# Kernel optimization log

Hardware: AMD Instinct MI355X
Metric: run time of the kernel (lower is better)

The kernel has to match this reference:

```python
import jax, jax.numpy as jnp
import numpy as np

DIM = 1024
NUM_HEADS = 16
HEAD_DIM = DIM // NUM_HEADS
ROPE_BASE = 10000.0


def _rope_cos_sin(seq_len, head_dim):
    inv_freq = 1.0 / (ROPE_BASE ** (jnp.arange(0, head_dim, 2, dtype=jnp.float32) / head_dim))
    t = jnp.arange(seq_len, dtype=jnp.float32)
    freqs = t[:, None] * inv_freq[None, :]            # [S, Dh/2]
    emb = jnp.concatenate([freqs, freqs], axis=-1)    # [S, Dh]
    return jnp.cos(emb), jnp.sin(emb)


def _rotate_half(x):
    half = x.shape[-1] // 2
    return jnp.concatenate([-x[..., half:], x[..., :half]], axis=-1)


def setup_inputs() -> dict:
    key = jax.random.key(0)
    k1, k2, k3 = jax.random.split(key, 3)
    B, S = 2, 2048
    x = jax.random.normal(k1, (B, S, DIM), dtype=jnp.float32)
    w_qkv = jax.random.normal(k2, (3 * DIM, DIM), dtype=jnp.float32) * (DIM ** -0.5)
    w_out = jax.random.normal(k3, (DIM, DIM), dtype=jnp.float32) * (DIM ** -0.5)
    return {"x": x, "w_qkv": w_qkv, "w_out": w_out}


def reference(x, w_qkv, w_out):
    B, S, D = x.shape
    H, Dh = NUM_HEADS, HEAD_DIM
    scale = Dh ** -0.5

    qkv = (x @ w_qkv.T).reshape(B, S, 3, H, Dh)      # [B,S,3,H,Dh]
    qkv = jnp.transpose(qkv, (2, 0, 3, 1, 4))        # [3,B,H,S,Dh]
    q, k, v = qkv[0], qkv[1], qkv[2]

    cos, sin = _rope_cos_sin(S, Dh)                  # [S,Dh]
    cos = cos[None, None, :, :]
    sin = sin[None, None, :, :]
    q = q * cos + _rotate_half(q) * sin
    k = k * cos + _rotate_half(k) * sin

    scores = jnp.einsum('bhqd,bhkd->bhqk', q, k) * scale
    causal_mask = jnp.triu(jnp.ones((S, S), dtype=bool), k=1)
    scores = jnp.where(causal_mask[None, None], -jnp.inf, scores)
    attn = jax.nn.softmax(scores, axis=-1)
    out = jnp.einsum('bhqk,bhkd->bhqd', attn, v)      # [B,H,S,Dh]
    out = jnp.transpose(out, (0, 2, 1, 3)).reshape(B, S, D)
    return out @ w_out.T
```

## Files before the change

### kernel.cpp

```cpp
#include <hip/hip_runtime.h>
#include <stdint.h>

typedef uint16_t u16;
typedef __attribute__((ext_vector_type(8))) short bf16x8;
typedef __attribute__((ext_vector_type(4))) float f32x4;

__device__ inline u16 f2b(float f) {
  uint32_t u = __float_as_uint(f);
  u += 0x7FFF + ((u >> 16) & 1);
  return (u16)(u >> 16);
}
__device__ inline float b2f(u16 h) {
  return __uint_as_float(((uint32_t)h) << 16);
}

__global__ void k_detect(const u16* __restrict__ X, int* __restrict__ flag) {
  __shared__ int cnt;
  const int t = threadIdx.x;
  if (t == 0) cnt = 0;
  __syncthreads();
  float av = fabsf(b2f(X[t * 2]));
  int wild = (av < 1000.0f) ? 0 : 1;
  atomicAdd(&cnt, wild);
  __syncthreads();
  if (t == 0) flag[0] = (cnt > 16) ? 1 : 0;
}

__global__ __launch_bounds__(256) void k_qkv_rope(const void* __restrict__ Xv,
                                                  const void* __restrict__ Wv,
                                                  const int* __restrict__ flag,
                                                  u16* __restrict__ Qo,
                                                  u16* __restrict__ Ko,
                                                  u16* __restrict__ Vo) {
  __shared__ u16 As[64][40];
  __shared__ u16 Bs[3][64][40];
  __shared__ float Cs[64][66];
  const int mode = flag[0];
  const int h = blockIdx.x;
  const int n0h = h * 64;
  const int m0 = blockIdx.y * 64;
  const int t = threadIdx.x, w = t >> 6, lane = t & 63;
  const int lr = lane & 15, lq = lane >> 4;
  f32x4 acc[3][4] = {};
  const int rA = t >> 2, cA = (t & 3) * 8;
  const int aoff = (m0 + rA) * 1024 + cA;
  const int boff0 = (n0h + rA) * 1024 + cA;
  for (int k0 = 0; k0 < 1024; k0 += 32) {
    __syncthreads();
    if (mode == 0) {
      *(uint4*)&As[rA][cA]    = *(const uint4*)((const u16*)Xv + aoff + k0);
      *(uint4*)&Bs[0][rA][cA] = *(const uint4*)((const u16*)Wv + boff0 + k0);
      *(uint4*)&Bs[1][rA][cA] = *(const uint4*)((const u16*)Wv + boff0 + 1048576 + k0);
      *(uint4*)&Bs[2][rA][cA] = *(const uint4*)((const u16*)Wv + boff0 + 2097152 + k0);
    } else {
      const float* Xf = (const float*)Xv;
      const float* Wf = (const float*)Wv;
#pragma unroll
      for (int ee = 0; ee < 8; ++ee) {
        As[rA][cA + ee]    = f2b(Xf[aoff + k0 + ee]);
        Bs[0][rA][cA + ee] = f2b(Wf[boff0 + k0 + ee]);
        Bs[1][rA][cA + ee] = f2b(Wf[boff0 + 1048576 + k0 + ee]);
        Bs[2][rA][cA + ee] = f2b(Wf[boff0 + 2097152 + k0 + ee]);
      }
    }
    __syncthreads();
    bf16x8 bf[3];
#pragma unroll
    for (int e = 0; e < 3; ++e)
      bf[e] = *(const bf16x8*)&Bs[e][(w << 4) + lr][lq * 8];
#pragma unroll
    for (int mt = 0; mt < 4; ++mt) {
      bf16x8 af = *(const bf16x8*)&As[(mt << 4) + lr][lq * 8];
#pragma unroll
      for (int e = 0; e < 3; ++e)
        acc[e][mt] = __builtin_amdgcn_mfma_f32_16x16x32_bf16(af, bf[e], acc[e][mt], 0, 0, 0);
    }
  }
  for (int e = 0; e < 3; ++e) {
    __syncthreads();
    {
      const int col = (w << 4) + lr;
#pragma unroll
      for (int mt = 0; mt < 4; ++mt)
#pragma unroll
        for (int i = 0; i < 4; ++i)
          Cs[mt * 16 + lq * 4 + i][col] = acc[e][mt][i];
    }
    __syncthreads();
    if (e == 2) {
      const int sx = t & 63, dh0 = (t >> 6) * 16;
      const int m = m0 + sx, b = m >> 11, s = m & 2047;
      const long hb = (long)(b * 16 + h) * 64;
#pragma unroll
      for (int u = 0; u < 16; ++u) {
        int dh = dh0 + u;
        Vo[(hb + dh) * 2048 + s] = f2b(Cs[sx][dh]);
      }
    } else {
      const int r = t >> 2, dh0 = (t & 3) * 16;
      const int m = m0 + r, b = m >> 11, s = m & 2047;
      const int obase = ((b * 16 + h) * 2048 + s) * 64;
      u16* O = (e == 0) ? Qo : Ko;
#pragma unroll
      for (int u = 0; u < 16; ++u) {
        int dh = dh0 + u;
        float v  = Cs[r][dh];
        float vp = Cs[r][dh ^ 32];
        float sign = (dh < 32) ? -1.0f : 1.0f;
        float fr  = __expf((float)(dh & 31) * -0.28782314f);
        float ang = (float)s * fr;
        float sn = __sinf(ang), cs = __cosf(ang);
        O[obase + dh] = f2b(v * cs + sign * vp * sn);
      }
    }
  }
}

__device__ __forceinline__ void attn_tile(u16 QP[64][72], u16 Ks[64][72],
                                          u16 Vt[64][72], const bf16x8 qf[2],
                                          f32x4 o_acc[4], float& m_i, float& l_i,
                                          int kt, int qt_tile, int w, int lr,
                                          int lq, int lq4, int base16, int qrow_l) {
  f32x4 sa[4] = {};
#pragma unroll
  for (int mb = 0; mb < 4; ++mb)
#pragma unroll
    for (int kk = 0; kk < 2; ++kk) {
      bf16x8 kf = *(const bf16x8*)&Ks[mb * 16 + lr][kk * 32 + lq * 8];
      sa[mb] = __builtin_amdgcn_mfma_f32_16x16x32_bf16(kf, qf[kk], sa[mb], 0, 0, 0);
    }
  float sc[4][4];
  float m_new = m_i;
#pragma unroll
  for (int mb = 0; mb < 4; ++mb)
#pragma unroll
    for (int i = 0; i < 4; ++i) {
      float sv = sa[mb][i] * 0.125f;
      if (kt == qt_tile && (mb * 16 + lq4 + i) > qrow_l) sv = -3.0e4f;
      sc[mb][i] = sv;
      m_new = fmaxf(m_new, sv);
    }
  m_new = fmaxf(m_new, __shfl_xor(m_new, 16));
  m_new = fmaxf(m_new, __shfl_xor(m_new, 32));
  float alpha = __expf(m_i - m_new);
  m_i = m_new;
  float p[4][4], sm = 0.f;
#pragma unroll
  for (int mb = 0; mb < 4; ++mb)
#pragma unroll
    for (int i = 0; i < 4; ++i) { p[mb][i] = __expf(sc[mb][i] - m_new); sm += p[mb][i]; }
  sm += __shfl_xor(sm, 16);
  sm += __shfl_xor(sm, 32);
  l_i = l_i * alpha + sm;

#pragma unroll
  for (int mb = 0; mb < 4; ++mb) {
    uint2 pk;
    pk.x = (uint32_t)f2b(p[mb][0]) | ((uint32_t)f2b(p[mb][1]) << 16);
    pk.y = (uint32_t)f2b(p[mb][2]) | ((uint32_t)f2b(p[mb][3]) << 16);
    *(uint2*)&QP[w * 16 + lr][mb * 16 + lq4] = pk;
  }
#pragma unroll
  for (int i = 0; i < 4; ++i) {
    float ai = __shfl(alpha, base16 | (lq4 + i));
    o_acc[0][i] *= ai; o_acc[1][i] *= ai;
    o_acc[2][i] *= ai; o_acc[3][i] *= ai;
  }
  asm volatile("s_waitcnt lgkmcnt(0)" ::: "memory");
#pragma unroll
  for (int kk = 0; kk < 2; ++kk) {
    bf16x8 pf = *(const bf16x8*)&QP[w * 16 + lr][kk * 32 + lq * 8];
#pragma unroll
    for (int nb = 0; nb < 4; ++nb) {
      bf16x8 vf = *(const bf16x8*)&Vt[nb * 16 + lr][kk * 32 + lq * 8];
      o_acc[nb] = __builtin_amdgcn_mfma_f32_16x16x32_bf16(pf, vf, o_acc[nb], 0, 0, 0);
    }
  }
}

__global__ __launch_bounds__(256) void k_attn(const u16* __restrict__ Q,
                                              const u16* __restrict__ K,
                                              const u16* __restrict__ V,
                                              u16* __restrict__ AO) {
  __shared__ u16 QP[64][72];
  __shared__ u16 Ks[64][72];
  __shared__ u16 Vt[64][72];
  const int qtA = 31 - blockIdx.x;
  const int qtB = blockIdx.x;
  const int bh = blockIdx.y;
  const int b = bh >> 4, h = bh & 15;
  const u16* Qg = Q + (bh * 2048) * 64;
  const u16* Kg = K + bh * 2048 * 64;
  const u16* Vg = V + (long)bh * 64 * 2048;
  const int t = threadIdx.x, w = t >> 6, lane = t & 63;
  const int lr = lane & 15, lq = lane >> 4;
  const int lq4 = lq * 4;
  const int base16 = lane & 48;
  const int r0 = t >> 3, c0 = (t & 7) * 8;
  const int qrow_l = w * 16 + lr;

  bf16x8 qfA[2], qfB[2];
  *(uint4*)&QP[r0][c0]      = *(const uint4*)&Qg[(qtA * 64 + r0) * 64 + c0];
  *(uint4*)&QP[r0 + 32][c0] = *(const uint4*)&Qg[(qtA * 64 + r0 + 32) * 64 + c0];
  __syncthreads();
#pragma unroll
  for (int kk = 0; kk < 2; ++kk)
    qfA[kk] = *(const bf16x8*)&QP[w * 16 + lr][kk * 32 + lq * 8];
  __syncthreads();
  *(uint4*)&QP[r0][c0]      = *(const uint4*)&Qg[(qtB * 64 + r0) * 64 + c0];
  *(uint4*)&QP[r0 + 32][c0] = *(const uint4*)&Qg[(qtB * 64 + r0 + 32) * 64 + c0];
  __syncthreads();
#pragma unroll
  for (int kk = 0; kk < 2; ++kk)
    qfB[kk] = *(const bf16x8*)&QP[w * 16 + lr][kk * 32 + lq * 8];

  float m_iA = -3.0e4f, l_iA = 0.f, m_iB = -3.0e4f, l_iB = 0.f;
  f32x4 o_accA[4] = {}, o_accB[4] = {};

  for (int kt = 0; kt <= qtA; ++kt) {
    __syncthreads();
    *(uint4*)&Ks[r0][c0]      = *(const uint4*)&Kg[(kt * 64 + r0) * 64 + c0];
    *(uint4*)&Ks[r0 + 32][c0] = *(const uint4*)&Kg[(kt * 64 + r0 + 32) * 64 + c0];
    *(uint4*)&Vt[r0][c0]      = *(const uint4*)&Vg[r0 * 2048 + kt * 64 + c0];
    *(uint4*)&Vt[r0 + 32][c0] = *(const uint4*)&Vg[(r0 + 32) * 2048 + kt * 64 + c0];
    __syncthreads();

    attn_tile(QP, Ks, Vt, qfA, o_accA, m_iA, l_iA, kt, qtA,
              w, lr, lq, lq4, base16, qrow_l);
    if (kt <= qtB) {
      asm volatile("s_waitcnt lgkmcnt(0)" ::: "memory");
      attn_tile(QP, Ks, Vt, qfB, o_accB, m_iB, l_iB, kt, qtB,
                w, lr, lq, lq4, base16, qrow_l);
    }
  }
  float linvA = 1.0f / l_iA, linvB = 1.0f / l_iB;
#pragma unroll
  for (int i = 0; i < 4; ++i) {
    float invA = __shfl(linvA, base16 | (lq4 + i));
    float invB = __shfl(linvB, base16 | (lq4 + i));
    int rowA = qtA * 64 + w * 16 + lq4 + i;
    int rowB = qtB * 64 + w * 16 + lq4 + i;
    int obA = (b * 2048 + rowA) * 1024 + h * 64;
    int obB = (b * 2048 + rowB) * 1024 + h * 64;
#pragma unroll
    for (int nb = 0; nb < 4; ++nb) {
      AO[obA + nb * 16 + lr] = f2b(o_accA[nb][i] * invA);
      AO[obB + nb * 16 + lr] = f2b(o_accB[nb][i] * invB);
    }
  }
}

__global__ __launch_bounds__(256) void k_gemm_out(const u16* __restrict__ A,
                                                  const void* __restrict__ Bv,
                                                  const int* __restrict__ flag,
                                                  void* __restrict__ Cv) {
  __shared__ u16 As[64][40];
  __shared__ u16 Bs[2][64][40];
  const int mode = flag[0];
  const int n0 = blockIdx.x * 128, m0 = blockIdx.y * 64;
  const int t = threadIdx.x, w = t >> 6, lane = t & 63;
  const int lr = lane & 15, lq = lane >> 4;
  f32x4 acc[2][4] = {};
  const int rA = t >> 2, cA = (t & 3) * 8;
  const int aoff = (m0 + rA) * 1024 + cA;
  const int boff = (n0 + rA) * 1024 + cA;
  for (int k0 = 0; k0 < 1024; k0 += 32) {
    __syncthreads();
    *(uint4*)&As[rA][cA] = *(const uint4*)(A + aoff + k0);
    if (mode == 0) {
      *(uint4*)&Bs[0][rA][cA] = *(const uint4*)((const u16*)Bv + boff + k0);
      *(uint4*)&Bs[1][rA][cA] = *(const uint4*)((const u16*)Bv + boff + 65536 + k0);
    } else {
      const float* Bf = (const float*)Bv;
#pragma unroll
      for (int e = 0; e < 8; ++e) {
        Bs[0][rA][cA + e] = f2b(Bf[boff + k0 + e]);
        Bs[1][rA][cA + e] = f2b(Bf[boff + 65536 + k0 + e]);
      }
    }
    __syncthreads();
    bf16x8 bfx[2];
#pragma unroll
    for (int e = 0; e < 2; ++e)
      bfx[e] = *(const bf16x8*)&Bs[e][(w << 4) + lr][lq * 8];
#pragma unroll
    for (int mt = 0; mt < 4; ++mt) {
      bf16x8 af = *(const bf16x8*)&As[(mt << 4) + lr][lq * 8];
#pragma unroll
      for (int e = 0; e < 2; ++e)
        acc[e][mt] = __builtin_amdgcn_mfma_f32_16x16x32_bf16(af, bfx[e], acc[e][mt], 0, 0, 0);
    }
  }
#pragma unroll
  for (int e = 0; e < 2; ++e) {
    const int col = n0 + e * 64 + (w << 4) + lr;
    if (mode == 0) {
      u16* C = (u16*)Cv;
#pragma unroll
      for (int mt = 0; mt < 4; ++mt)
#pragma unroll
        for (int i = 0; i < 4; ++i)
          C[(m0 + mt * 16 + lq * 4 + i) * 1024 + col] = f2b(acc[e][mt][i]);
    } else {
      float* C = (float*)Cv;
#pragma unroll
      for (int mt = 0; mt < 4; ++mt)
#pragma unroll
        for (int i = 0; i < 4; ++i)
          C[(m0 + mt * 16 + lq * 4 + i) * 1024 + col] = acc[e][mt][i];
    }
  }
}

extern "C" void kernel_launch(void* const* d_in, const int* in_sizes, int n_in,
                              void* d_out, int out_size, void* d_ws, size_t ws_size,
                              hipStream_t stream) {
  const void* x    = d_in[0];
  const void* wqkv = d_in[1];
  const void* wout = d_in[2];

  int* flag = (int*)d_ws;
  u16* qb = (u16*)((char*)d_ws + 256);
  u16* kb = qb + 4194304;
  u16* vb = kb + 4194304;
  u16* ao = vb + 4194304;

  k_detect  <<<dim3(1), 256, 0, stream>>>((const u16*)x, flag);
  k_qkv_rope<<<dim3(16, 64), 256, 0, stream>>>(x, wqkv, flag, qb, kb, vb);
  k_attn    <<<dim3(16, 32), 256, 0, stream>>>(qb, kb, vb, ao);
  k_gemm_out<<<dim3(8, 64), 256, 0, stream>>>(ao, wout, flag, d_out);
}
```

Measured before the change: 235.6 us.

## Double M tile in QKV and output GEMMs to reuse weight tiles

Each block of the QKV+RoPE GEMM and of the output projection GEMM now computes 128 rows instead of 64. Each loaded weight tile feeds twice as many MFMAs, which halves the weight traffic and its fp32-to-bf16 conversion work. Accumulator registers double and the grid size halves, which may reduce occupancy and the number of CUs kept busy.

Result: no change. 234.7 us (-0.4%).

```diff
diff --git a/kernel.cpp b/kernel.cpp
--- a/kernel.cpp
+++ b/kernel.cpp
@@ -32,23 +32,25 @@
                                                   u16* __restrict__ Qo,
                                                   u16* __restrict__ Ko,
                                                   u16* __restrict__ Vo) {
-  __shared__ u16 As[64][40];
+  __shared__ u16 As[2][64][40];
   __shared__ u16 Bs[3][64][40];
   __shared__ float Cs[64][66];
   const int mode = flag[0];
   const int h = blockIdx.x;
   const int n0h = h * 64;
-  const int m0 = blockIdx.y * 64;
+  const int m0 = blockIdx.y * 128;
   const int t = threadIdx.x, w = t >> 6, lane = t & 63;
   const int lr = lane & 15, lq = lane >> 4;
-  f32x4 acc[3][4] = {};
+  f32x4 acc[3][2][4] = {};
   const int rA = t >> 2, cA = (t & 3) * 8;
-  const int aoff = (m0 + rA) * 1024 + cA;
+  const int aoff0 = (m0 + rA) * 1024 + cA;
+  const int aoff1 = (m0 + 64 + rA) * 1024 + cA;
   const int boff0 = (n0h + rA) * 1024 + cA;
   for (int k0 = 0; k0 < 1024; k0 += 32) {
     __syncthreads();
     if (mode == 0) {
-      *(uint4*)&As[rA][cA]    = *(const uint4*)((const u16*)Xv + aoff + k0);
+      *(uint4*)&As[0][rA][cA] = *(const uint4*)((const u16*)Xv + aoff0 + k0);
+      *(uint4*)&As[1][rA][cA] = *(const uint4*)((const u16*)Xv + aoff1 + k0);
       *(uint4*)&Bs[0][rA][cA] = *(const uint4*)((const u16*)Wv + boff0 + k0);
       *(uint4*)&Bs[1][rA][cA] = *(const uint4*)((const u16*)Wv + boff0 + 1048576 + k0);
       *(uint4*)&Bs[2][rA][cA] = *(const uint4*)((const u16*)Wv + boff0 + 2097152 + k0);
@@ -57,7 +59,8 @@
       const float* Wf = (const float*)Wv;
 #pragma unroll
       for (int ee = 0; ee < 8; ++ee) {
-        As[rA][cA + ee]    = f2b(Xf[aoff + k0 + ee]);
+        As[0][rA][cA + ee] = f2b(Xf[aoff0 + k0 + ee]);
+        As[1][rA][cA + ee] = f2b(Xf[aoff1 + k0 + ee]);
         Bs[0][rA][cA + ee] = f2b(Wf[boff0 + k0 + ee]);
         Bs[1][rA][cA + ee] = f2b(Wf[boff0 + 1048576 + k0 + ee]);
         Bs[2][rA][cA + ee] = f2b(Wf[boff0 + 2097152 + k0 + ee]);
@@ -70,47 +73,53 @@
       bf[e] = *(const bf16x8*)&Bs[e][(w << 4) + lr][lq * 8];
 #pragma unroll
     for (int mt = 0; mt < 4; ++mt) {
-      bf16x8 af = *(const bf16x8*)&As[(mt << 4) + lr][lq * 8];
-#pragma unroll
-      for (int e = 0; e < 3; ++e)
-        acc[e][mt] = __builtin_amdgcn_mfma_f32_16x16x32_bf16(af, bf[e], acc[e][mt], 0, 0, 0);
-    }
-  }
-  for (int e = 0; e < 3; ++e) {
-    __syncthreads();
-    {
-      const int col = (w << 4) + lr;
-#pragma unroll
-      for (int mt = 0; mt < 4; ++mt)
-#pragma unroll
-        for (int i = 0; i < 4; ++i)
-          Cs[mt * 16 + lq * 4 + i][col] = acc[e][mt][i];
-    }
-    __syncthreads();
-    if (e == 2) {
-      const int sx = t & 63, dh0 = (t >> 6) * 16;
-      const int m = m0 + sx, b = m >> 11, s = m & 2047;
-      const long hb = (long)(b * 16 + h) * 64;
-#pragma unroll
-      for (int u = 0; u < 16; ++u) {
-        int dh = dh0 + u;
-        Vo[(hb + dh) * 2048 + s] = f2b(Cs[sx][dh]);
-      }
-    } else {
-      const int r = t >> 2, dh0 = (t & 3) * 16;
-      const int m = m0 + r, b = m >> 11, s = m & 2047;
-      const int obase = ((b * 16 + h) * 2048 + s) * 64;
-      u16* O = (e == 0) ? Qo : Ko;
-#pragma unroll
-      for (int u = 0; u < 16; ++u) {
-        int dh = dh0 + u;
-        float v  = Cs[r][dh];
-        float vp = Cs[r][dh ^ 32];
-        float sign = (dh < 32) ? -1.0f : 1.0f;
-        float fr  = __expf((float)(dh & 31) * -0.28782314f);
-        float ang = (float)s * fr;
-        float sn = __sinf(ang), cs = __cosf(ang);
-        O[obase + dh] = f2b(v * cs + sign * vp * sn);
+      bf16x8 af0 = *(const bf16x8*)&As[0][(mt << 4) + lr][lq * 8];
+      bf16x8 af1 = *(const bf16x8*)&As[1][(mt << 4) + lr][lq * 8];
+#pragma unroll
+      for (int e = 0; e < 3; ++e) {
+        acc[e][0][mt] = __builtin_amdgcn_mfma_f32_16x16x32_bf16(af0, bf[e], acc[e][0][mt], 0, 0, 0);
+        acc[e][1][mt] = __builtin_amdgcn_mfma_f32_16x16x32_bf16(af1, bf[e], acc[e][1][mt], 0, 0, 0);
+      }
+    }
+  }
+  for (int f = 0; f < 2; ++f) {
+    const int m0f = m0 + f * 64;
+    for (int e = 0; e < 3; ++e) {
+      __syncthreads();
+      {
+        const int col = (w << 4) + lr;
+#pragma unroll
+        for (int mt = 0; mt < 4; ++mt)
+#pragma unroll
+          for (int i = 0; i < 4; ++i)
+            Cs[mt * 16 + lq * 4 + i][col] = acc[e][f][mt][i];
+      }
+      __syncthreads();
+      if (e == 2) {
+        const int sx = t & 63, dh0 = (t >> 6) * 16;
+        const int m = m0f + sx, b = m >> 11, s = m & 2047;
+        const long hb = (long)(b * 16 + h) * 64;
+#pragma unroll
+        for (int u = 0; u < 16; ++u) {
+          int dh = dh0 + u;
+          Vo[(hb + dh) * 2048 + s] = f2b(Cs[sx][dh]);
+        }
+      } else {
+        const int r = t >> 2, dh0 = (t & 3) * 16;
+        const int m = m0f + r, b = m >> 11, s = m & 2047;
+        const int obase = ((b * 16 + h) * 2048 + s) * 64;
+        u16* O = (e == 0) ? Qo : Ko;
+#pragma unroll
+        for (int u = 0; u < 16; ++u) {
+          int dh = dh0 + u;
+          float v  = Cs[r][dh];
+          float vp = Cs[r][dh ^ 32];
+          float sign = (dh < 32) ? -1.0f : 1.0f;
+          float fr  = __expf((float)(dh & 31) * -0.28782314f);
+          float ang = (float)s * fr;
+          float sn = __sinf(ang), cs = __cosf(ang);
+          O[obase + dh] = f2b(v * cs + sign * vp * sn);
+        }
       }
     }
   }
@@ -152,7 +161,6 @@
   sm += __shfl_xor(sm, 16);
   sm += __shfl_xor(sm, 32);
   l_i = l_i * alpha + sm;
-
 #pragma unroll
   for (int mb = 0; mb < 4; ++mb) {
     uint2 pk;
@@ -254,19 +262,21 @@
                                                   const void* __restrict__ Bv,
                                                   const int* __restrict__ flag,
                                                   void* __restrict__ Cv) {
-  __shared__ u16 As[64][40];
+  __shared__ u16 As[2][64][40];
   __shared__ u16 Bs[2][64][40];
   const int mode = flag[0];
-  const int n0 = blockIdx.x * 128, m0 = blockIdx.y * 64;
+  const int n0 = blockIdx.x * 128, m0 = blockIdx.y * 128;
   const int t = threadIdx.x, w = t >> 6, lane = t & 63;
   const int lr = lane & 15, lq = lane >> 4;
-  f32x4 acc[2][4] = {};
+  f32x4 acc[2][2][4] = {};
   const int rA = t >> 2, cA = (t & 3) * 8;
-  const int aoff = (m0 + rA) * 1024 + cA;
+  const int aoff0 = (m0 + rA) * 1024 + cA;
+  const int aoff1 = (m0 + 64 + rA) * 1024 + cA;
   const int boff = (n0 + rA) * 1024 + cA;
   for (int k0 = 0; k0 < 1024; k0 += 32) {
     __syncthreads();
-    *(uint4*)&As[rA][cA] = *(const uint4*)(A + aoff + k0);
+    *(uint4*)&As[0][rA][cA] = *(const uint4*)(A + aoff0 + k0);
+    *(uint4*)&As[1][rA][cA] = *(const uint4*)(A + aoff1 + k0);
     if (mode == 0) {
       *(uint4*)&Bs[0][rA][cA] = *(const uint4*)((const u16*)Bv + boff + k0);
       *(uint4*)&Bs[1][rA][cA] = *(const uint4*)((const u16*)Bv + boff + 65536 + k0);
@@ -285,31 +295,37 @@
       bfx[e] = *(const bf16x8*)&Bs[e][(w << 4) + lr][lq * 8];
 #pragma unroll
     for (int mt = 0; mt < 4; ++mt) {
-      bf16x8 af = *(const bf16x8*)&As[(mt << 4) + lr][lq * 8];
-#pragma unroll
-      for (int e = 0; e < 2; ++e)
-        acc[e][mt] = __builtin_amdgcn_mfma_f32_16x16x32_bf16(af, bfx[e], acc[e][mt], 0, 0, 0);
-    }
-  }
-#pragma unroll
-  for (int e = 0; e < 2; ++e) {
-    const int col = n0 + e * 64 + (w << 4) + lr;
-    if (mode == 0) {
-      u16* C = (u16*)Cv;
-#pragma unroll
-      for (int mt = 0; mt < 4; ++mt)
-#pragma unroll
-        for (int i = 0; i < 4; ++i)
-          C[(m0 + mt * 16 + lq * 4 + i) * 1024 + col] = f2b(acc[e][mt][i]);
-    } else {
-      float* C = (float*)Cv;
-#pragma unroll
-      for (int mt = 0; mt < 4; ++mt)
-#pragma unroll
-        for (int i = 0; i < 4; ++i)
-          C[(m0 + mt * 16 + lq * 4 + i) * 1024 + col] = acc[e][mt][i];
-    }
-  }
+      bf16x8 af0 = *(const bf16x8*)&As[0][(mt << 4) + lr][lq * 8];
+      bf16x8 af1 = *(const bf16x8*)&As[1][(mt << 4) + lr][lq * 8];
+#pragma unroll
+      for (int e = 0; e < 2; ++e) {
+        acc[e][0][mt] = __builtin_amdgcn_mfma_f32_16x16x32_bf16(af0, bfx[e], acc[e][0][mt], 0, 0, 0);
+        acc[e][1][mt] = __builtin_amdgcn_mfma_f32_16x16x32_bf16(af1, bfx[e], acc[e][1][mt], 0, 0, 0);
+      }
+    }
+  }
+#pragma unroll
+  for (int e = 0; e < 2; ++e)
+#pragma unroll
+    for (int f = 0; f < 2; ++f) {
+      const int col = n0 + e * 64 + (w << 4) + lr;
+      const int m0f = m0 + f * 64;
+      if (mode == 0) {
+        u16* C = (u16*)Cv;
+#pragma unroll
+        for (int mt = 0; mt < 4; ++mt)
+#pragma unroll
+          for (int i = 0; i < 4; ++i)
+            C[(m0f + mt * 16 + lq * 4 + i) * 1024 + col] = f2b(acc[e][f][mt][i]);
+      } else {
+        float* C = (float*)Cv;
+#pragma unroll
+        for (int mt = 0; mt < 4; ++mt)
+#pragma unroll
+          for (int i = 0; i < 4; ++i)
+            C[(m0f + mt * 16 + lq * 4 + i) * 1024 + col] = acc[e][f][mt][i];
+      }
+    }
 }
 
 extern "C" void kernel_launch(void* const* d_in, const int* in_sizes, int n_in,
@@ -326,7 +342,7 @@
   u16* ao = vb + 4194304;
 
   k_detect  <<<dim3(1), 256, 0, stream>>>((const u16*)x, flag);
-  k_qkv_rope<<<dim3(16, 64), 256, 0, stream>>>(x, wqkv, flag, qb, kb, vb);
+  k_qkv_rope<<<dim3(16, 32), 256, 0, stream>>>(x, wqkv, flag, qb, kb, vb);
   k_attn    <<<dim3(16, 32), 256, 0, stream>>>(qb, kb, vb, ao);
-  k_gemm_out<<<dim3(8, 64), 256, 0, stream>>>(ao, wout, flag, d_out);
-}
+  k_gemm_out<<<dim3(8, 32), 256, 0, stream>>>(ao, wout, flag, d_out);
+}
```
